# Optimization experiments

Hardware: AMD Instinct MI355X
Metric: run time of the kernel (lower is better)

## Reference

```python
import jax, jax.numpy as jnp
import numpy as np

N = 50000
D = 512
H = 128
C = 32
E1 = 1600000
E2 = 3200000


def gcn_conv(x, W, b, src, dst, n_nodes):
    """PyG GCNConv: linear transform, add self-loops, symmetric norm, scatter-add, bias."""
    loop = jnp.arange(n_nodes, dtype=src.dtype)
    src = jnp.concatenate([src, loop])
    dst = jnp.concatenate([dst, loop])
    deg = jax.ops.segment_sum(jnp.ones_like(dst, dtype=x.dtype), dst, num_segments=n_nodes)
    dinv = jnp.where(deg > 0, jax.lax.rsqrt(deg), 0.0)
    norm = dinv[src] * dinv[dst]                    # [E+N]
    h = x @ W                                       # [N, out] dense GEMM first (PyG order)
    msg = h[src] * norm[:, None]                    # gather + scale, [E+N, out]
    out = jax.ops.segment_sum(msg, dst, num_segments=n_nodes)
    return out + b


def setup_inputs() -> dict:
    key = jax.random.key(0)
    ks = jax.random.split(key, 9)
    x = jax.random.normal(ks[0], (N, D), dtype=jnp.float32)
    edge_index = jax.random.randint(ks[1], (2, E1), 0, N, dtype=jnp.int64)
    sec_edge_index = jax.random.randint(ks[2], (2, E2), 0, N, dtype=jnp.int64)
    s1 = 1.0 / np.sqrt(D)
    s3 = 1.0 / np.sqrt(2 * H)
    W1 = jax.random.uniform(ks[3], (D, H), jnp.float32, -s1, s1)
    b1 = jnp.zeros((H,), jnp.float32)
    W2 = jax.random.uniform(ks[4], (D, H), jnp.float32, -s1, s1)
    b2 = jnp.zeros((H,), jnp.float32)
    W3 = jax.random.uniform(ks[5], (2 * H, C), jnp.float32, -s3, s3)
    b3 = jnp.zeros((C,), jnp.float32)
    return {"x": x, "edge_index": edge_index, "sec_edge_index": sec_edge_index,
            "W1": W1, "b1": b1, "W2": W2, "b2": b2, "W3": W3, "b3": b3}


def reference(x, edge_index, sec_edge_index, W1, b1, W2, b2, W3, b3):
    src1, dst1 = edge_index[0], edge_index[1]
    src2, dst2 = sec_edge_index[0], sec_edge_index[1]
    h1 = gcn_conv(x, W1, b1, src1, dst1, N)          # [N, H]
    h2 = gcn_conv(x, W2, b2, src2, dst2, N)          # [N, H]
    h = jax.nn.relu(jnp.concatenate([h1, h2], axis=-1))  # [N, 2H]
    # dropout is identity in eval mode
    out = gcn_conv(h, W3, b3, src1, dst1, N)         # [N, C]
    return jax.nn.log_softmax(out, axis=1)
```

## Files before the change

kernel.cpp:

```cpp
#include <hip/hip_runtime.h>

#define NNODES 50000
#define DIM 512
#define HID 128
#define NCLS 32
#define NBINS 196
#define CHUNK 8192
#define AGG_WAVES_G1 2048
#define AGG_WAVES_G2 4096
#define A3_WAVES 4096
#define HS_SCALE 64.0f
#define HS_ISCALE 0.015625f

typedef __attribute__((ext_vector_type(8))) short bf16x8;
typedef __attribute__((ext_vector_type(4))) float f32x4;
typedef __attribute__((ext_vector_type(2))) float f32x2;

__device__ __forceinline__ unsigned short f2bf(float f) {
    union { float f; unsigned int u; } a; a.f = f;
    unsigned int u = a.u;
    u += 0x7fff + ((u >> 16) & 1);
    return (unsigned short)(u >> 16);
}
__device__ __forceinline__ float bf2f(unsigned short h) {
    union { unsigned int u; float f; } a; a.u = ((unsigned int)h) << 16;
    return a.f;
}
__device__ __forceinline__ unsigned char f2fp8(float f) {
    int p = __builtin_amdgcn_cvt_pk_fp8_f32(f, 0.f, 0, false);
    return (unsigned char)(p & 0xff);
}
__device__ __forceinline__ void fp8add2(unsigned int u, f32x2& a01, f32x2& a23) {
    a01 += __builtin_amdgcn_cvt_pk_f32_fp8((int)u, false);
    a23 += __builtin_amdgcn_cvt_pk_f32_fp8((int)u, true);
}
__device__ __forceinline__ int lbound(const int* __restrict__ rp, int q) {
    int lo = 0, hi = NNODES;
    while (lo < hi) { int mid = (lo + hi) >> 1; if (rp[mid] >= q) hi = mid; else lo = mid + 1; }
    return lo;
}
__device__ __forceinline__ void scan_inplace(int* __restrict__ row, int n, int* __restrict__ total) {
    __shared__ int wsum[4];
    int tid = threadIdx.x, lane = tid & 63, wid = tid >> 6;
    int base = 0;
    for (int start = 0; start < n; start += 256) {
        int i = start + tid;
        int v = (i < n) ? row[i] : 0;
        int x = v;
        #pragma unroll
        for (int off = 1; off < 64; off <<= 1) {
            int t = __shfl_up(x, off);
            if (lane >= off) x += t;
        }
        if (lane == 63) wsum[wid] = x;
        __syncthreads();
        int woff = 0, tot = 0;
        #pragma unroll
        for (int w = 0; w < 4; ++w) { int s = wsum[w]; if (w < wid) woff += s; tot += s; }
        __syncthreads();
        if (i < n) row[i] = base + woff + x - v;
        base += tot;
    }
    if (tid == 0) *total = base;
}


__global__ __launch_bounds__(256)
void hist2_kernel(const int* __restrict__ dst1, int E1, int nb1, int* __restrict__ hist1,
                  const int* __restrict__ dst2, int E2, int nb2, int* __restrict__ hist2) {
    __shared__ int h[NBINS];
    int blk = blockIdx.x;
    const int* dst; int E, nb, b; int* hist;
    if (blk < nb1) { dst = dst1; E = E1; nb = nb1; b = blk; hist = hist1; }
    else { dst = dst2; E = E2; nb = nb2; b = blk - nb1; hist = hist2; }
    int tid = threadIdx.x;
    for (int i = tid; i < NBINS; i += 256) h[i] = 0;
    __syncthreads();
    int e0 = b * CHUNK;
    int e1 = min(E, e0 + CHUNK);
    for (int e = e0 + tid; e < e1; e += 256)
        atomicAdd(&h[dst[e] >> 8], 1);
    __syncthreads();
    for (int i = tid; i < NBINS; i += 256)
        hist[(size_t)i * nb + b] = h[i];
}

__global__ __launch_bounds__(256)
void scanrow2_kernel(int* __restrict__ hist1, int nb1, int* __restrict__ bs1,
                     int* __restrict__ hist2, int nb2, int* __restrict__ bs2) {
    int b = blockIdx.x;
    if (b < NBINS) scan_inplace(hist1 + (size_t)b * nb1, nb1, bs1 + b);
    else           scan_inplace(hist2 + (size_t)(b - NBINS) * nb2, nb2, bs2 + (b - NBINS));
}

__global__ __launch_bounds__(256)
void scanbs_kernel(int* __restrict__ bs1, int* __restrict__ bs2) {
    if (blockIdx.x == 0) scan_inplace(bs1, NBINS, bs1 + NBINS);
    else                 scan_inplace(bs2, NBINS, bs2 + NBINS);
}

__global__ __launch_bounds__(256)
void scatter2_kernel(const int* __restrict__ src1, const int* __restrict__ dst1, int E1, int nb1,
                     const int* __restrict__ hist1, const int* __restrict__ bs1,
                     unsigned int* __restrict__ binned1,
                     const int* __restrict__ src2, const int* __restrict__ dst2, int E2, int nb2,
                     const int* __restrict__ hist2, const int* __restrict__ bs2,
                     unsigned int* __restrict__ binned2) {
    __shared__ int cur[NBINS];
    int blk = blockIdx.x;
    const int *src, *dst, *hist, *bs; int E, nb, b; unsigned int* binned;
    if (blk < nb1) { src = src1; dst = dst1; E = E1; nb = nb1; b = blk; hist = hist1; bs = bs1; binned = binned1; }
    else { src = src2; dst = dst2; E = E2; nb = nb2; b = blk - nb1; hist = hist2; bs = bs2; binned = binned2; }
    int tid = threadIdx.x;
    for (int i = tid; i < NBINS; i += 256)
        cur[i] = hist[(size_t)i * nb + b] + bs[i];
    __syncthreads();
    int e0 = b * CHUNK;
    int e1 = min(E, e0 + CHUNK);
    for (int e = e0 + tid; e < e1; e += 256) {
        int d = dst[e];
        int bb = d >> 8;
        int p = atomicAdd(&cur[bb], 1);
        binned[p] = ((unsigned int)(d & 255) << 16) | (unsigned int)src[e];
    }
}

__global__ __launch_bounds__(256)
void binfill2_kernel(const unsigned int* __restrict__ binned1, const int* __restrict__ bs1,
                     int* __restrict__ rowptr1, float* __restrict__ dinv1,
                     int* __restrict__ col1, int E1,
                     const unsigned int* __restrict__ binned2, const int* __restrict__ bs2,
                     int* __restrict__ rowptr2, float* __restrict__ dinv2,
                     int* __restrict__ col2, int E2) {
    __shared__ int cnt[256], cur[256];
    __shared__ int wsum[4];
    int b = blockIdx.x;
    const unsigned int* binned; const int* bs; int* rowptr; float* dinv; int* col; int totalE;
    if (b < NBINS) { binned = binned1; bs = bs1; rowptr = rowptr1; dinv = dinv1; col = col1; totalE = E1; }
    else { b -= NBINS; binned = binned2; bs = bs2; rowptr = rowptr2; dinv = dinv2; col = col2; totalE = E2; }
    int tid = threadIdx.x, lane = tid & 63, wid = tid >> 6;
    int s = bs[b], e = bs[b + 1];
    cnt[tid] = 0;
    __syncthreads();
    for (int i = s + tid; i < e; i += 256)
        atomicAdd(&cnt[binned[i] >> 16], 1);
    __syncthreads();
    int v = cnt[tid];
    int x = v;
    #pragma unroll
    for (int off = 1; off < 64; off <<= 1) {
        int t = __shfl_up(x, off);
        if (lane >= off) x += t;
    }
    if (lane == 63) wsum[wid] = x;
    __syncthreads();
    int woff = 0;
    #pragma unroll
    for (int w = 0; w < 4; ++w) if (w < wid) woff += wsum[w];
    int ex = woff + x - v;
    cur[tid] = ex;
    __syncthreads();
    int node = b * 256 + tid;
    if (node < NNODES) {
        rowptr[node] = s + ex;
        dinv[node] = rsqrtf((float)v + 1.0f);
    }
    if (b == 0 && tid == 0) rowptr[NNODES] = totalE;
    for (int i = s + tid; i < e; i += 256) {
        unsigned int pk = binned[i];
        int ld = pk >> 16;
        int p = atomicAdd(&cur[ld], 1);
        col[s + p] = (int)(pk & 0xffff);
    }
}


__global__ __launch_bounds__(256)
void convW_kernel(const float* __restrict__ W1, const float* __restrict__ W2,
                  unsigned short* __restrict__ Wt2) {
    int k = blockIdx.x;
    int c = threadIdx.x;
    float v = (c < HID) ? W1[(size_t)k * HID + c] : W2[(size_t)k * HID + (c - HID)];
    int kt = k >> 5, kg = (k >> 3) & 3, kidx = k & 7;
    Wt2[(size_t)kt * 8192 + kg * 2048 + c * 8 + kidx] = f2bf(v);
}


__global__ __launch_bounds__(256)
void convW3_kernel(const float* __restrict__ W3, unsigned short* __restrict__ Wt3) {
    int idx = blockIdx.x * 256 + threadIdx.x;
    int k = idx >> 5, c = idx & 31;
    int kt = k >> 5, kg = (k >> 3) & 3, kidx = k & 7;
    Wt3[(kt * 4 + kg) * 256 + c * 8 + kidx] = f2bf(W3[(size_t)k * NCLS + c]);
}


__global__ __launch_bounds__(256)
void gemm12_mfma_kernel(const float* __restrict__ x, const unsigned short* __restrict__ Wt2,
                        const float* __restrict__ dinv1, const float* __restrict__ dinv2,
                        unsigned char* __restrict__ hs8) {
    __shared__ unsigned short Bs[2][8192];
    int tid = threadIdx.x;
    int wv = tid >> 6, l = tid & 63;
    int lr = l & 15, lg = l >> 4;
    int m0 = blockIdx.x * 64;
    int row = m0 + wv * 16 + lr;
    int rowc = min(row, NNODES - 1);
    const float* xrow = x + (size_t)rowc * DIM;

    f32x4 acc[16];
    #pragma unroll
    for (int n = 0; n < 16; ++n) acc[n] = (f32x4){0.f, 0.f, 0.f, 0.f};

    uint4 bn[4];
    float4 a0, a1, a0n, a1n;
    #pragma unroll
    for (int p = 0; p < 4; ++p)
        bn[p] = *(const uint4*)(Wt2 + p * 2048 + tid * 8);
    a0 = *(const float4*)(xrow + lg * 8);
    a1 = *(const float4*)(xrow + lg * 8 + 4);
    #pragma unroll
    for (int p = 0; p < 4; ++p)
        *(uint4*)(&Bs[0][p * 2048 + tid * 8]) = bn[p];
    __syncthreads();

    int cur = 0;
    for (int kt = 0; kt < 16; ++kt) {
        if (kt < 15) {
            #pragma unroll
            for (int p = 0; p < 4; ++p)
                bn[p] = *(const uint4*)(Wt2 + (size_t)(kt + 1) * 8192 + p * 2048 + tid * 8);
            a0n = *(const float4*)(xrow + (kt + 1) * 32 + lg * 8);
            a1n = *(const float4*)(xrow + (kt + 1) * 32 + lg * 8 + 4);
        }
        union { bf16x8 v; unsigned short u[8]; } af;
        af.u[0] = f2bf(a0.x); af.u[1] = f2bf(a0.y);
        af.u[2] = f2bf(a0.z); af.u[3] = f2bf(a0.w);
        af.u[4] = f2bf(a1.x); af.u[5] = f2bf(a1.y);
        af.u[6] = f2bf(a1.z); af.u[7] = f2bf(a1.w);
        #pragma unroll
        for (int nf = 0; nf < 16; ++nf) {
            bf16x8 bf = *(const bf16x8*)(&Bs[cur][lg * 2048 + (nf * 16 + lr) * 8]);
            acc[nf] = __builtin_amdgcn_mfma_f32_16x16x32_bf16(af.v, bf, acc[nf], 0, 0, 0);
        }
        if (kt < 15) {
            #pragma unroll
            for (int p = 0; p < 4; ++p)
                *(uint4*)(&Bs[cur ^ 1][p * 2048 + tid * 8]) = bn[p];
            __syncthreads();
            cur ^= 1;
            a0 = a0n; a1 = a1n;
        }
    }

    int row0 = m0 + wv * 16 + lg * 4;
    float d1[4], d2[4];
    #pragma unroll
    for (int j = 0; j < 4; ++j) {
        bool ok = (row0 + j) < NNODES;
        d1[j] = ok ? dinv1[row0 + j] * HS_SCALE : 0.f;
        d2[j] = ok ? dinv2[row0 + j] * HS_SCALE : 0.f;
    }
    #pragma unroll
    for (int nf = 0; nf < 16; ++nf) {
        int c = nf * 16 + lr;
        const float* d = (nf < 8) ? d1 : d2;
        #pragma unroll
        for (int j = 0; j < 4; ++j) {
            int r = row0 + j;
            if (r < NNODES)
                hs8[(size_t)r * 256 + c] = f2fp8(acc[nf][j] * d[j]);
        }
    }
}


__global__ __launch_bounds__(256)
void agg12_kernel(const unsigned char* __restrict__ hs8,
                  const int* __restrict__ rowptr1, const int* __restrict__ col1,
                  const int* __restrict__ rowptr2, const int* __restrict__ col2,
                  const float* __restrict__ dinv1, const float* __restrict__ dinv2,
                  const float* __restrict__ b1, const float* __restrict__ b2,
                  int E1, int E2, unsigned short* __restrict__ hcat) {
    int gw = blockIdx.x * 4 + (threadIdx.x >> 6);
    int lane = threadIdx.x & 63;
    int g, w, W; long long E;
    const int *rowptr, *col; const float *dinv, *bias;
    if (gw < AGG_WAVES_G1) {
        g = 0; w = gw; W = AGG_WAVES_G1; E = E1;
        rowptr = rowptr1; col = col1; dinv = dinv1; bias = b1;
    } else {
        g = 1; w = gw - AGG_WAVES_G1; W = AGG_WAVES_G2; E = E2;
        rowptr = rowptr2; col = col2; dinv = dinv2; bias = b2;
    }
    int q0 = (int)(E * w / W);
    int q1 = (int)(E * (w + 1) / W);
    int v0 = lbound(rowptr, q0);
    int v1 = (w == W - 1) ? NNODES : lbound(rowptr, q1);

    int quarter = lane >> 4;
    int lc = lane & 15;
    float bias8[8];
    #pragma unroll
    for (int j = 0; j < 8; ++j) bias8[j] = bias[lc * 8 + j];
    const unsigned char* hsg = hs8 + g * 128;

    for (int v = v0; v < v1; ++v) {
        int e0 = rowptr[v], e1 = rowptr[v + 1];
        f32x2 acc[4];
        #pragma unroll
        for (int i = 0; i < 4; ++i) acc[i] = (f32x2){0.f, 0.f};
        int e = e0;
        #pragma unroll 2
        for (; e + 8 <= e1; e += 8) {
            int sA = col[e + quarter];
            int sB = col[e + 4 + quarter];
            uint2 uA = *(const uint2*)(hsg + (size_t)sA * 256 + lc * 8);
            uint2 uB = *(const uint2*)(hsg + (size_t)sB * 256 + lc * 8);
            fp8add2(uA.x, acc[0], acc[1]); fp8add2(uA.y, acc[2], acc[3]);
            fp8add2(uB.x, acc[0], acc[1]); fp8add2(uB.y, acc[2], acc[3]);
        }
        if (e + 4 <= e1) {
            int sA = col[e + quarter];
            uint2 uA = *(const uint2*)(hsg + (size_t)sA * 256 + lc * 8);
            fp8add2(uA.x, acc[0], acc[1]); fp8add2(uA.y, acc[2], acc[3]);
            e += 4;
        }
        if (e < e1 && quarter < e1 - e) {
            int sA = col[e + quarter];
            uint2 uA = *(const uint2*)(hsg + (size_t)sA * 256 + lc * 8);
            fp8add2(uA.x, acc[0], acc[1]); fp8add2(uA.y, acc[2], acc[3]);
        }
        #pragma unroll
        for (int i = 0; i < 4; ++i) {
            #pragma unroll
            for (int off = 16; off <= 32; off <<= 1) {
                acc[i][0] += __shfl_xor(acc[i][0], off);
                acc[i][1] += __shfl_xor(acc[i][1], off);
            }
        }
        uint2 su = *(const uint2*)(hsg + (size_t)v * 256 + lc * 8);
        fp8add2(su.x, acc[0], acc[1]); fp8add2(su.y, acc[2], acc[3]);
        float sc = dinv[v] * HS_ISCALE;
        if (quarter == 0) {
            unsigned int res[4];
            #pragma unroll
            for (int p = 0; p < 4; ++p) {
                float r0 = fmaxf(acc[p][0] * sc + bias8[2 * p + 0], 0.f);
                float r1 = fmaxf(acc[p][1] * sc + bias8[2 * p + 1], 0.f);
                res[p] = (unsigned int)f2bf(r0) | ((unsigned int)f2bf(r1) << 16);
            }
            uint4 st = {res[0], res[1], res[2], res[3]};
            *(uint4*)(hcat + (size_t)v * 256 + g * 128 + lc * 8) = st;
        }
    }
}


__global__ __launch_bounds__(256)
void gemm3_mfma_kernel(const unsigned short* __restrict__ hcat,
                       const unsigned short* __restrict__ Wt3,
                       const float* __restrict__ dinv1, unsigned short* __restrict__ gs) {
    __shared__ unsigned short Ws[8192];
    int tid = threadIdx.x;
    #pragma unroll
    for (int p = 0; p < 4; ++p)
        *(uint4*)(&Ws[p * 2048 + tid * 8]) = *(const uint4*)(Wt3 + p * 2048 + tid * 8);
    __syncthreads();

    int wv = tid >> 6, l = tid & 63;
    int lr = l & 15, lg = l >> 4;
    int rbase = blockIdx.x * 256 + wv * 64;

    f32x4 acc[4][2];
    #pragma unroll
    for (int m = 0; m < 4; ++m)
        #pragma unroll
        for (int n = 0; n < 2; ++n)
            acc[m][n] = (f32x4){0.f, 0.f, 0.f, 0.f};

    #pragma unroll
    for (int kt = 0; kt < 8; ++kt) {
        #pragma unroll
        for (int m = 0; m < 4; ++m) {
            int rA = min(rbase + m * 16 + lr, NNODES - 1);
            bf16x8 af = *(const bf16x8*)(hcat + (size_t)rA * 256 + kt * 32 + lg * 8);
            #pragma unroll
            for (int n = 0; n < 2; ++n) {
                bf16x8 bf = *(const bf16x8*)(&Ws[(kt * 4 + lg) * 256 + (n * 16 + lr) * 8]);
                acc[m][n] = __builtin_amdgcn_mfma_f32_16x16x32_bf16(af, bf, acc[m][n], 0, 0, 0);
            }
        }
    }

    #pragma unroll
    for (int m = 0; m < 4; ++m) {
        int row0 = rbase + m * 16 + lg * 4;
        float d[4];
        #pragma unroll
        for (int j = 0; j < 4; ++j)
            d[j] = (row0 + j < NNODES) ? dinv1[row0 + j] : 0.f;
        #pragma unroll
        for (int n = 0; n < 2; ++n) {
            int c = n * 16 + lr;
            #pragma unroll
            for (int j = 0; j < 4; ++j) {
                int r = row0 + j;
                if (r < NNODES)
                    gs[(size_t)r * 32 + c] = f2bf(acc[m][n][j] * d[j]);
            }
        }
    }
}


__global__ __launch_bounds__(256)
void agg3_kernel(const unsigned short* __restrict__ gs, const int* __restrict__ rowptr1,
                 const int* __restrict__ col1, const float* __restrict__ dinv1,
                 const float* __restrict__ b3, float* __restrict__ out, int E1) {
    int gw = blockIdx.x * 4 + (threadIdx.x >> 6);
    int lane = threadIdx.x & 63;
    long long E = E1;
    int q0 = (int)(E * gw / A3_WAVES);
    int q1 = (int)(E * (gw + 1) / A3_WAVES);
    int v0 = lbound(rowptr1, q0);
    int v1 = (gw == A3_WAVES - 1) ? NNODES : lbound(rowptr1, q1);

    int oct = lane >> 3;
    int lc = lane & 7;
    float4 b3v = *(const float4*)(b3 + lc * 4);

    for (int v = v0; v < v1; ++v) {
        int e0 = rowptr1[v], e1 = rowptr1[v + 1];
        float a0 = 0.f, a1 = 0.f, a2 = 0.f, a3 = 0.f;
        int e = e0;
        #pragma unroll 2
        for (; e + 8 <= e1; e += 8) {
            int srco = col1[e + oct];
            uint2 u = *(const uint2*)(gs + (size_t)srco * 32 + lc * 4);
            a0 += bf2f((unsigned short)(u.x & 0xffff));
            a1 += bf2f((unsigned short)(u.x >> 16));
            a2 += bf2f((unsigned short)(u.y & 0xffff));
            a3 += bf2f((unsigned short)(u.y >> 16));
        }
        if (e < e1) {
            int r = e1 - e;
            if (oct < r) {
                int srco = col1[e + oct];
                uint2 u = *(const uint2*)(gs + (size_t)srco * 32 + lc * 4);
                a0 += bf2f((unsigned short)(u.x & 0xffff));
                a1 += bf2f((unsigned short)(u.x >> 16));
                a2 += bf2f((unsigned short)(u.y & 0xffff));
                a3 += bf2f((unsigned short)(u.y >> 16));
            }
        }
        #pragma unroll
        for (int off = 32; off >= 8; off >>= 1) {
            a0 += __shfl_xor(a0, off); a1 += __shfl_xor(a1, off);
            a2 += __shfl_xor(a2, off); a3 += __shfl_xor(a3, off);
        }
        uint2 su = *(const uint2*)(gs + (size_t)v * 32 + lc * 4);
        a0 += bf2f((unsigned short)(su.x & 0xffff));
        a1 += bf2f((unsigned short)(su.x >> 16));
        a2 += bf2f((unsigned short)(su.y & 0xffff));
        a3 += bf2f((unsigned short)(su.y >> 16));
        float d = dinv1[v];
        float l0 = a0 * d + b3v.x, l1 = a1 * d + b3v.y;
        float l2 = a2 * d + b3v.z, l3 = a3 * d + b3v.w;
        float m = fmaxf(fmaxf(l0, l1), fmaxf(l2, l3));
        #pragma unroll
        for (int off = 1; off <= 4; off <<= 1) m = fmaxf(m, __shfl_xor(m, off));
        float s = expf(l0 - m) + expf(l1 - m) + expf(l2 - m) + expf(l3 - m);
        #pragma unroll
        for (int off = 1; off <= 4; off <<= 1) s += __shfl_xor(s, off);
        float lg = logf(s);
        if (oct == 0) {
            float4 o = make_float4(l0 - m - lg, l1 - m - lg, l2 - m - lg, l3 - m - lg);
            *(float4*)(out + (size_t)v * 32 + lc * 4) = o;
        }
    }
}

extern "C" void kernel_launch(void* const* d_in, const int* in_sizes, int n_in,
                              void* d_out, int out_size, void* d_ws, size_t ws_size,
                              hipStream_t stream) {
    const float* x  = (const float*)d_in[0];
    const int* ei1  = (const int*)d_in[1];
    const int* ei2  = (const int*)d_in[2];
    const float* W1 = (const float*)d_in[3];
    const float* b1 = (const float*)d_in[4];
    const float* W2 = (const float*)d_in[5];
    const float* b2 = (const float*)d_in[6];
    const float* W3 = (const float*)d_in[7];
    const float* b3 = (const float*)d_in[8];
    float* out = (float*)d_out;

    int E1 = in_sizes[1] / 2;
    int E2 = in_sizes[2] / 2;
    const int* src1 = ei1;       const int* dst1 = ei1 + E1;
    const int* src2 = ei2;       const int* dst2 = ei2 + E2;
    int nb1 = (E1 + CHUNK - 1) / CHUNK;
    int nb2 = (E2 + CHUNK - 1) / CHUNK;

    char* w = (char*)d_ws;
    auto alloc = [&](size_t bytes) -> char* {
        char* p = w; w += (bytes + 255) & ~(size_t)255; return p;
    };
    int* hist1   = (int*)alloc((size_t)NBINS * nb1 * 4);
    int* hist2   = (int*)alloc((size_t)NBINS * nb2 * 4);
    int* bs1     = (int*)alloc((size_t)(NBINS + 1) * 4);
    int* bs2     = (int*)alloc((size_t)(NBINS + 1) * 4);
    int* rowptr1 = (int*)alloc((size_t)(NNODES + 1) * 4);
    int* rowptr2 = (int*)alloc((size_t)(NNODES + 1) * 4);
    float* dinv1 = (float*)alloc((size_t)NNODES * 4);
    float* dinv2 = (float*)alloc((size_t)NNODES * 4);
    int* col1    = (int*)alloc((size_t)E1 * 4);
    int* col2    = (int*)alloc((size_t)E2 * 4);
    unsigned short* Wt2 = (unsigned short*)alloc((size_t)256 * DIM * 2);
    unsigned short* Wt3 = (unsigned short*)alloc((size_t)256 * NCLS * 2);
    unsigned char* hs8 = (unsigned char*)alloc((size_t)NNODES * 256);
    unsigned short* gs = (unsigned short*)alloc((size_t)NNODES * 32 * 2);
    unsigned short* hcat = (unsigned short*)alloc((size_t)NNODES * 256 * 2);
    unsigned int* binned1 = (unsigned int*)hcat;
    unsigned int* binned2 = binned1 + E1;

    hist2_kernel<<<nb1 + nb2, 256, 0, stream>>>(dst1, E1, nb1, hist1, dst2, E2, nb2, hist2);
    scanrow2_kernel<<<NBINS * 2, 256, 0, stream>>>(hist1, nb1, bs1, hist2, nb2, bs2);
    scanbs_kernel<<<2, 256, 0, stream>>>(bs1, bs2);
    scatter2_kernel<<<nb1 + nb2, 256, 0, stream>>>(src1, dst1, E1, nb1, hist1, bs1, binned1,
                                                   src2, dst2, E2, nb2, hist2, bs2, binned2);
    binfill2_kernel<<<NBINS * 2, 256, 0, stream>>>(binned1, bs1, rowptr1, dinv1, col1, E1,
                                                   binned2, bs2, rowptr2, dinv2, col2, E2);

    convW_kernel<<<DIM, 256, 0, stream>>>(W1, W2, Wt2);
    convW3_kernel<<<32, 256, 0, stream>>>(W3, Wt3);
    gemm12_mfma_kernel<<<(NNODES + 63) / 64, 256, 0, stream>>>(x, Wt2, dinv1, dinv2, hs8);
    agg12_kernel<<<(AGG_WAVES_G1 + AGG_WAVES_G2) / 4, 256, 0, stream>>>(
        hs8, rowptr1, col1, rowptr2, col2, dinv1, dinv2, b1, b2, E1, E2, hcat);
    gemm3_mfma_kernel<<<(NNODES + 255) / 256, 256, 0, stream>>>(hcat, Wt3, dinv1, gs);
    agg3_kernel<<<A3_WAVES / 4, 256, 0, stream>>>(gs, rowptr1, col1, dinv1, b3, out, E1);
}
```

Before: 323.1 us.

## Use direct global-to-LDS loads in GEMM, merge weight-convert kernels, retune aggregation waves

The first GEMM now stages each weight tile with global_load_lds, which writes straight into shared memory instead of going through registers and a separate LDS store. The intent is to save VGPRs and instructions in the double-buffered loop. The two weight-conversion kernels are merged into one launch to cut launch overhead. The wave counts for the layer-1/2 aggregation kernel are also raised, which changes how much work each wave gets and how many waves are resident. Direct-to-LDS loads depend on per-lane LDS addresses being laid out as the hardware expects and on the compiler inserting the right waits before the barrier.

```diff
diff --git a/kernel.cpp b/kernel.cpp
--- a/kernel.cpp
+++ b/kernel.cpp
@@ -6,8 +6,8 @@
 #define NCLS 32
 #define NBINS 196
 #define CHUNK 8192
-#define AGG_WAVES_G1 2048
-#define AGG_WAVES_G2 4096
+#define AGG_WAVES_G1 2728
+#define AGG_WAVES_G2 5464
 #define A3_WAVES 4096
 #define HS_SCALE 64.0f
 #define HS_ISCALE 0.015625f
@@ -177,21 +177,20 @@
 
 __global__ __launch_bounds__(256)
 void convW_kernel(const float* __restrict__ W1, const float* __restrict__ W2,
-                  unsigned short* __restrict__ Wt2) {
-    int k = blockIdx.x;
-    int c = threadIdx.x;
-    float v = (c < HID) ? W1[(size_t)k * HID + c] : W2[(size_t)k * HID + (c - HID)];
-    int kt = k >> 5, kg = (k >> 3) & 3, kidx = k & 7;
-    Wt2[(size_t)kt * 8192 + kg * 2048 + c * 8 + kidx] = f2bf(v);
-}
-
-
-__global__ __launch_bounds__(256)
-void convW3_kernel(const float* __restrict__ W3, unsigned short* __restrict__ Wt3) {
-    int idx = blockIdx.x * 256 + threadIdx.x;
-    int k = idx >> 5, c = idx & 31;
-    int kt = k >> 5, kg = (k >> 3) & 3, kidx = k & 7;
-    Wt3[(kt * 4 + kg) * 256 + c * 8 + kidx] = f2bf(W3[(size_t)k * NCLS + c]);
+                  const float* __restrict__ W3,
+                  unsigned short* __restrict__ Wt2, unsigned short* __restrict__ Wt3) {
+    if (blockIdx.x < DIM) {
+        int k = blockIdx.x;
+        int c = threadIdx.x;
+        float v = (c < HID) ? W1[(size_t)k * HID + c] : W2[(size_t)k * HID + (c - HID)];
+        int kt = k >> 5, kg = (k >> 3) & 3, kidx = k & 7;
+        Wt2[(size_t)kt * 8192 + kg * 2048 + c * 8 + kidx] = f2bf(v);
+    } else {
+        int idx = (blockIdx.x - DIM) * 256 + threadIdx.x;
+        int k = idx >> 5, c = idx & 31;
+        int kt = k >> 5, kg = (k >> 3) & 3, kidx = k & 7;
+        Wt3[(kt * 4 + kg) * 256 + c * 8 + kidx] = f2bf(W3[(size_t)k * NCLS + c]);
+    }
 }
 
 
@@ -212,24 +211,26 @@
     #pragma unroll
     for (int n = 0; n < 16; ++n) acc[n] = (f32x4){0.f, 0.f, 0.f, 0.f};
 
-    uint4 bn[4];
+    auto stage = [&](int kt, int buf) {
+        const unsigned short* srcb = Wt2 + (size_t)kt * 8192 + tid * 8;
+        #pragma unroll
+        for (int p = 0; p < 4; ++p) {
+            __builtin_amdgcn_global_load_lds(
+                (const __attribute__((address_space(1))) unsigned int*)(const void*)(srcb + p * 2048),
+                (__attribute__((address_space(3))) unsigned int*)(void*)(&Bs[buf][p * 2048 + tid * 8]),
+                16, 0, 0);
+        }
+    };
+
     float4 a0, a1, a0n, a1n;
-    #pragma unroll
-    for (int p = 0; p < 4; ++p)
-        bn[p] = *(const uint4*)(Wt2 + p * 2048 + tid * 8);
+    stage(0, 0);
     a0 = *(const float4*)(xrow + lg * 8);
     a1 = *(const float4*)(xrow + lg * 8 + 4);
-    #pragma unroll
-    for (int p = 0; p < 4; ++p)
-        *(uint4*)(&Bs[0][p * 2048 + tid * 8]) = bn[p];
-    __syncthreads();
-
-    int cur = 0;
+    __syncthreads();
+
     for (int kt = 0; kt < 16; ++kt) {
         if (kt < 15) {
-            #pragma unroll
-            for (int p = 0; p < 4; ++p)
-                bn[p] = *(const uint4*)(Wt2 + (size_t)(kt + 1) * 8192 + p * 2048 + tid * 8);
+            stage(kt + 1, (kt + 1) & 1);
             a0n = *(const float4*)(xrow + (kt + 1) * 32 + lg * 8);
             a1n = *(const float4*)(xrow + (kt + 1) * 32 + lg * 8 + 4);
         }
@@ -240,15 +241,11 @@
         af.u[6] = f2bf(a1.z); af.u[7] = f2bf(a1.w);
         #pragma unroll
         for (int nf = 0; nf < 16; ++nf) {
-            bf16x8 bf = *(const bf16x8*)(&Bs[cur][lg * 2048 + (nf * 16 + lr) * 8]);
+            bf16x8 bf = *(const bf16x8*)(&Bs[kt & 1][lg * 2048 + (nf * 16 + lr) * 8]);
             acc[nf] = __builtin_amdgcn_mfma_f32_16x16x32_bf16(af.v, bf, acc[nf], 0, 0, 0);
         }
         if (kt < 15) {
-            #pragma unroll
-            for (int p = 0; p < 4; ++p)
-                *(uint4*)(&Bs[cur ^ 1][p * 2048 + tid * 8]) = bn[p];
             __syncthreads();
-            cur ^= 1;
             a0 = a0n; a1 = a1n;
         }
     }
@@ -532,8 +529,7 @@
     binfill2_kernel<<<NBINS * 2, 256, 0, stream>>>(binned1, bs1, rowptr1, dinv1, col1, E1,
                                                    binned2, bs2, rowptr2, dinv2, col2, E2);
 
-    convW_kernel<<<DIM, 256, 0, stream>>>(W1, W2, Wt2);
-    convW3_kernel<<<32, 256, 0, stream>>>(W3, Wt3);
+    convW_kernel<<<DIM + 32, 256, 0, stream>>>(W1, W2, W3, Wt2, Wt3);
     gemm12_mfma_kernel<<<(NNODES + 63) / 64, 256, 0, stream>>>(x, Wt2, dinv1, dinv2, hs8);
     agg12_kernel<<<(AGG_WAVES_G1 + AGG_WAVES_G2) / 4, 256, 0, stream>>>(
         hs8, rowptr1, col1, rowptr2, col2, dinv1, dinv2, b1, b2, E1, E2, hcat);
```

Result: no change. 319.0 us (-1.3%).
